# Performance work log

Hardware: AMD Instinct MI355X
Metric: run time of the kernel (lower is better)

Reference implementation:

```python
import math
import jax, jax.numpy as jnp
import numpy as np

B, K, D, R = 8192, 64, 128, 8
EPSILON = 1.0  # alpha_scale, used as diffusion epsilon


def setup_inputs() -> dict:
    key = jax.random.key(0)
    k1, k2, k3 = jax.random.split(key, 3)
    y = jax.random.normal(k1, (B, D), dtype=jnp.float32)
    m = 0.2 * jax.random.normal(k2, (K, D), dtype=jnp.float32)          # init_mean_scale=0.2
    delta = jnp.full((K, D), -2.0, dtype=jnp.float32)                    # init_delta=-2.0
    U = 0.001 * jax.random.normal(k3, (K, D, R), dtype=jnp.float32)
    # log_alpha_raw = alpha_scale * log(ones(K)/K)
    log_alpha_raw = jnp.full((K,), math.log(1.0 / K), dtype=jnp.float32)
    return {"y": y, "m": m, "delta": delta, "U": U, "log_alpha_raw": log_alpha_raw}


def reference(y, m, delta, U, log_alpha_raw):
    """log z_theta(y) = logsumexp_k [log_alpha_k + log N(y; m_k, eps*S_k)],
    S_k = diag(exp(delta_k)) + U_k U_k^T, solved via Woodbury + Cholesky."""
    d = y.shape[-1]
    eps = jnp.asarray(EPSILON, y.dtype)
    log_alpha = (log_alpha_raw - jnp.mean(log_alpha_raw)) / EPSILON

    S_diag = jnp.exp(delta)            # [K, d]
    S_inv = 1.0 / S_diag               # [K, d]

    # Capacitance M_k = I_r + U_k^T diag(S_inv_k) U_k, Cholesky L_k
    V = S_inv[..., None] * U                              # [K, d, r]
    Mcap = jnp.eye(R, dtype=y.dtype) + jnp.einsum('kdr,kds->krs', U, V)  # [K, r, r]
    L = jnp.linalg.cholesky(Mcap)                         # [K, r, r]
    logdet_S = jnp.sum(jnp.log(S_diag), axis=-1) \
        + 2.0 * jnp.sum(jnp.log(jnp.diagonal(L, axis1=-2, axis2=-1)), axis=-1)  # [K]

    diff = y[:, None, :] - m[None, :, :]                  # [B, K, d]
    u1 = diff * S_inv[None]                               # [B, K, d]
    # Woodbury correction: solve M_k s = U_k^T u1 for all (b, k)
    t = jnp.einsum('kdr,bkd->krb', U, u1)                 # [K, r, B] (B as multiple RHS)
    z1 = jax.scipy.linalg.solve_triangular(L, t, lower=True)
    s = jax.scipy.linalg.solve_triangular(jnp.swapaxes(L, -1, -2), z1, lower=False)  # [K, r, B]
    Us = jnp.einsum('kdr,krb->bkd', U, s)                 # [B, K, d]
    S_inv_diff = u1 - Us * S_inv[None]                    # [B, K, d]

    quad = jnp.sum(diff * S_inv_diff, axis=-1)            # [B, K]
    log_norm = 0.5 * (d * (math.log(2.0 * math.pi) + jnp.log(eps)) + logdet_S)  # [K]
    logits = log_alpha[None, :] - 0.5 * quad / eps - log_norm[None, :]          # [B, K]
    return jax.scipy.special.logsumexp(logits, axis=-1)   # [B]
```

## Files before the change

### kernel.cpp

```cpp
#include <hip/hip_runtime.h>
#include <math.h>

#define D_DIM 128
#define K_DIM 64
#define R_DIM 8
#define B_DIM 8192
#define KG    4
#define ESTR  161
#define TCH   5120

#define WS_C0F   81920
#define WS_PARTF 81984
#define WS_XGF   147520

typedef __bf16 bf16x8 __attribute__((ext_vector_type(8)));
typedef float  f32x4  __attribute__((ext_vector_type(4)));

static __device__ inline unsigned short f2bf(float f) {
  union { float f; unsigned int u; } v; v.f = f;
  unsigned int u = v.u;
  unsigned int lsb = (u >> 16) & 1;
  u += 0x7fffu + lsb;
  return (unsigned short)(u >> 16);
}

__global__ __launch_bounds__(128) void precomp_kernel(
    const float* __restrict__ m, const float* __restrict__ delta,
    const float* __restrict__ U, const float* __restrict__ lar,
    float* __restrict__ ws) {
  const int k = blockIdx.x;
  const int d = threadIdx.x;

  __shared__ float U_l[D_DIM][R_DIM];
  __shared__ float V_l[D_DIM][R_DIM];
  __shared__ float W_l[D_DIM][R_DIM];
  __shared__ float m_l[D_DIM];
  __shared__ float red[64];
  __shared__ float Linv_s[R_DIM][R_DIM];
  __shared__ float q_s[R_DIM];
  __shared__ float c0_s[1];
  __shared__ float redA[D_DIM], redB[D_DIM], redC[D_DIM];

  const float dl    = delta[k * D_DIM + d];
  const float s_inv = expf(-dl);
  const float mv    = m[k * D_DIM + d];
  m_l[d] = mv;
  const float* Up = U + (size_t)(k * D_DIM + d) * R_DIM;
#pragma unroll
  for (int r = 0; r < R_DIM; ++r) {
    float u = Up[r];
    U_l[d][r] = u;
    V_l[d][r] = u * s_inv;
  }
  redA[d] = dl;
  redB[d] = mv * mv * s_inv;
  redC[d] = (d < K_DIM) ? lar[d] : 0.f;
  __syncthreads();

  if (d < 64) {
    const int r = d >> 3, s = d & 7;
    float acc = (r == s) ? 1.0f : 0.0f;
#pragma unroll 8
    for (int dd = 0; dd < D_DIM; ++dd) acc += U_l[dd][r] * V_l[dd][s];
    red[d] = acc;
  }
  __syncthreads();

  for (int off = 64; off > 0; off >>= 1) {
    if (d < off) {
      redA[d] += redA[d + off];
      redB[d] += redB[d + off];
      redC[d] += redC[d + off];
    }
    __syncthreads();
  }

  if (d == 0) {
    float Lm[8][8];
#pragma unroll
    for (int i = 0; i < 8; ++i) {
#pragma unroll
      for (int j = 0; j < 8; ++j) {
        if (j > i) continue;
        float sum = red[i * 8 + j];
#pragma unroll
        for (int p = 0; p < 8; ++p)
          if (p < j) sum -= Lm[i][p] * Lm[j][p];
        if (i == j) Lm[i][i] = sqrtf(sum);
        else        Lm[i][j] = sum / Lm[j][j];
      }
    }
    float ld = 0.f;
#pragma unroll
    for (int i = 0; i < 8; ++i) ld += logf(Lm[i][i]);

    float Li[8][8];
#pragma unroll
    for (int i = 0; i < 8; ++i)
#pragma unroll
      for (int j = 0; j < 8; ++j) Li[i][j] = 0.f;
#pragma unroll
    for (int j = 0; j < 8; ++j) {
      Li[j][j] = 1.0f / Lm[j][j];
#pragma unroll
      for (int i = 0; i < 8; ++i) {
        if (i <= j) continue;
        float sum = 0.f;
#pragma unroll
        for (int p = 0; p < 8; ++p)
          if (p >= j && p < i) sum += Lm[i][p] * Li[p][j];
        Li[i][j] = -sum / Lm[i][i];
      }
    }
#pragma unroll
    for (int i = 0; i < 8; ++i)
#pragma unroll
      for (int j = 0; j < 8; ++j) Linv_s[i][j] = Li[i][j];

    const float mean = redC[0] * (1.0f / K_DIM);
    const float log_alpha = lar[k] - mean;
    const float logdetS = redA[0] + 2.0f * ld;
    const float LOG2PI = 1.8378770664093453f;
    const float log_norm = 0.5f * ((float)D_DIM * LOG2PI + logdetS);
    c0_s[0] = log_alpha - log_norm - 0.5f * redB[0];
  }
  __syncthreads();

  float Wr[R_DIM];
#pragma unroll
  for (int r = 0; r < R_DIM; ++r) {
    float acc = 0.f;
#pragma unroll
    for (int s2 = 0; s2 < R_DIM; ++s2)
      if (s2 <= r) acc += V_l[d][s2] * Linv_s[r][s2];
    Wr[r] = acc;
    W_l[d][r] = acc;
  }
  __syncthreads();

  if (d < R_DIM) {
    float acc = 0.f;
#pragma unroll 8
    for (int dd = 0; dd < D_DIM; ++dd) acc += W_l[dd][d] * m_l[dd];
    q_s[d] = acc;
  }
  __syncthreads();

  float hp = mv * s_inv;
#pragma unroll
  for (int r = 0; r < R_DIM; ++r) hp -= q_s[r] * Wr[r];

  const float INV_SQRT2 = 0.70710678118654752f;
  unsigned short* T = (unsigned short*)ws;
  const int kg = k >> 4, kl = k & 15;
  const int chunk = d >> 5, pos = d & 31;
  const size_t base_y = (((size_t)kg * 8 + chunk) * 160) * 32;
  const size_t base_q = (((size_t)kg * 8 + 4 + chunk) * 160) * 32;
#pragma unroll
  for (int c = 0; c < 8; ++c) {
    T[base_y + (size_t)(kl * 10 + c) * 32 + pos] = f2bf(Wr[c] * INV_SQRT2);
    T[base_q + (size_t)(kl * 10 + c) * 32 + pos] = 0;
  }
  T[base_y + (size_t)(kl * 10 + 8) * 32 + pos] = f2bf(hp);
  T[base_q + (size_t)(kl * 10 + 8) * 32 + pos] = f2bf(-0.5f * s_inv);
  T[base_y + (size_t)(kl * 10 + 9) * 32 + pos] = 0;
  T[base_q + (size_t)(kl * 10 + 9) * 32 + pos] = 0;

  if (d == 0) {
    float qq = 0.f;
#pragma unroll
    for (int r = 0; r < R_DIM; ++r) qq += q_s[r] * q_s[r];
    ws[WS_C0F + k] = c0_s[0] + 0.5f * qq;
  }
}

__global__ __launch_bounds__(256) void x_prep_kernel(
    const float* __restrict__ y, float* __restrict__ ws) {
  const int i   = blockIdx.x * 256 + threadIdx.x;
  const int row = i >> 5;
  const int seg = i & 31;
  const float4* ya = (const float4*)y + (size_t)row * 32 + (seg & 15) * 2;
  float4 a = ya[0], b = ya[1];
  if (seg >= 16) {
    a.x *= a.x; a.y *= a.y; a.z *= a.z; a.w *= a.w;
    b.x *= b.x; b.y *= b.y; b.z *= b.z; b.w *= b.w;
  }
  union { unsigned short us[8]; uint4 v; } o;
  o.us[0] = f2bf(a.x); o.us[1] = f2bf(a.y); o.us[2] = f2bf(a.z); o.us[3] = f2bf(a.w);
  o.us[4] = f2bf(b.x); o.us[5] = f2bf(b.y); o.us[6] = f2bf(b.z); o.us[7] = f2bf(b.w);
  uint4* xg = (uint4*)(ws + WS_XGF);
  xg[(size_t)row * 32 + (seg ^ (row & 31))] = o.v;
}

__global__ __launch_bounds__(256, 4) void logz_main(
    const float* __restrict__ ws, float* __restrict__ part) {
  __shared__ __align__(16) unsigned short sX[32 * 256];
  __shared__ __align__(16) float sbuf[32 * ESTR];
  __shared__ float vals2[32 * 17];

  const int tid   = threadIdx.x;
  const int lane  = tid & 63;
  const int wv    = tid >> 6;
  const int wr    = wv >> 1;
  const int wc    = wv & 1;
  const int col_l = lane & 15;
  const int quad  = lane >> 4;
  const int rt    = (int)blockIdx.x >> 2;
  const int kg    = (int)blockIdx.x & 3;

  {
    const float* xsrc = ws + WS_XGF + (size_t)rt * 4096;
#pragma unroll
    for (int j = 0; j < 4; ++j) {
      const int off = (wv * 4 + j) * 256;
      __builtin_amdgcn_global_load_lds(
          (const __attribute__((address_space(1))) void*)(xsrc + off + lane * 4),
          (__attribute__((address_space(3))) void*)((float*)sX + off),
          16, 0, 0);
    }
  }

  f32x4 acc[5];
#pragma unroll
  for (int f = 0; f < 5; ++f) { acc[f][0] = 0.f; acc[f][1] = 0.f; acc[f][2] = 0.f; acc[f][3] = 0.f; }

  const float* tG = ws + (size_t)kg * 8 * (TCH / 2);
  unsigned short* sT = (unsigned short*)sbuf;
  const int rowA = wr * 16 + col_l;

  for (int pair = 0; pair < 4; ++pair) {
    if (pair) __syncthreads();
    {
      const float* src = tG + (size_t)pair * TCH;
#pragma unroll
      for (int j = 0; j < 5; ++j) {
        const int off = (wv * 5 + j) * 256;
        __builtin_amdgcn_global_load_lds(
            (const __attribute__((address_space(1))) void*)(src + off + lane * 4),
            (__attribute__((address_space(3))) void*)((float*)sbuf + off),
            16, 0, 0);
      }
    }
    __syncthreads();
#pragma unroll
    for (int ii = 0; ii < 2; ++ii) {
      const int kiter = pair * 2 + ii;
      const bf16x8 a = *(const bf16x8*)(sX + ((size_t)rowA * 32
                          + (((kiter * 4 + quad) ^ rowA) & 31)) * 8);
      const unsigned short* cb = sT + ii * TCH;
#pragma unroll
      for (int f = 0; f < 5; ++f) {
        const bf16x8 b = *(const bf16x8*)(cb + (wc * 80 + f * 16 + col_l) * 32
                                             + quad * 8);
        acc[f] = __builtin_amdgcn_mfma_f32_16x16x32_bf16(a, b, acc[f], 0, 0, 0);
      }
    }
  }

  __syncthreads();
  float* evals = sbuf;
#pragma unroll
  for (int f = 0; f < 5; ++f) {
    const int col = wc * 80 + f * 16 + col_l;
    const int c10 = col % 10;
#pragma unroll
    for (int reg = 0; reg < 4; ++reg) {
      const float v = acc[f][reg];
      evals[(wr * 16 + quad * 4 + reg) * ESTR + col] = (c10 == 8) ? v : v * v;
    }
  }
  __syncthreads();

  const float* c0p = ws + WS_C0F + kg * 16;
#pragma unroll
  for (int j = 0; j < 2; ++j) {
    const int idx = tid + j * 256;
    const int row = idx >> 4, kl = idx & 15;
    const float* e = evals + row * ESTR + kl * 10;
    float s = c0p[kl] + e[8];
#pragma unroll
    for (int c = 0; c < 8; ++c) s += e[c];
    vals2[row * 17 + kl] = s;
  }
  __syncthreads();

  if (tid < 32) {
    const int row = tid;
    float mx = -INFINITY;
#pragma unroll
    for (int j = 0; j < 16; ++j) mx = fmaxf(mx, vals2[row * 17 + j]);
    float s = 0.f;
#pragma unroll
    for (int j = 0; j < 16; ++j) s += expf(vals2[row * 17 + j] - mx);
    *(float2*)(part + ((size_t)(rt * 32 + row) * KG + kg) * 2) = make_float2(mx, s);
  }
}

__global__ __launch_bounds__(256) void reduce_kernel(
    const float* __restrict__ part, float* __restrict__ out) {
  const int b = blockIdx.x * 256 + threadIdx.x;
  const float4 a0 = ((const float4*)part)[b * 2];
  const float4 a1 = ((const float4*)part)[b * 2 + 1];
  float mx = fmaxf(fmaxf(a0.x, a0.z), fmaxf(a1.x, a1.z));
  float s = a0.y * expf(a0.x - mx) + a0.w * expf(a0.z - mx)
          + a1.y * expf(a1.x - mx) + a1.w * expf(a1.z - mx);
  out[b] = mx + logf(s);
}

extern "C" void kernel_launch(void* const* d_in, const int* in_sizes, int n_in,
                              void* d_out, int out_size, void* d_ws, size_t ws_size,
                              hipStream_t stream) {
  const float* y     = (const float*)d_in[0];
  const float* m     = (const float*)d_in[1];
  const float* delta = (const float*)d_in[2];
  const float* U     = (const float*)d_in[3];
  const float* lar   = (const float*)d_in[4];
  float* out = (float*)d_out;
  float* ws  = (float*)d_ws;

  precomp_kernel<<<K_DIM, 128, 0, stream>>>(m, delta, U, lar, ws);
  x_prep_kernel<<<B_DIM * 32 / 256, 256, 0, stream>>>(y, ws);
  logz_main<<<(B_DIM / 32) * KG, 256, 0, stream>>>(ws, ws + WS_PARTF);
  reduce_kernel<<<B_DIM / 256, 256, 0, stream>>>(ws + WS_PARTF, out);
}
```

Measured before the change: 84.81 us.

## Fuse x-prep, main GEMM and logsumexp reduction into one kernel

```diff
diff --git a/kernel.cpp b/kernel.cpp
--- a/kernel.cpp
+++ b/kernel.cpp
@@ -5,13 +5,9 @@
 #define K_DIM 64
 #define R_DIM 8
 #define B_DIM 8192
-#define KG    4
-#define ESTR  161
-#define TCH   5120
+#define XSTR  264
 
 #define WS_C0F   81920
-#define WS_PARTF 81984
-#define WS_XGF   147520
 
 typedef __bf16 bf16x8 __attribute__((ext_vector_type(8)));
 typedef float  f32x4  __attribute__((ext_vector_type(4)));
@@ -174,137 +170,129 @@
   }
 }
 
-__global__ __launch_bounds__(256) void x_prep_kernel(
-    const float* __restrict__ y, float* __restrict__ ws) {
-  const int i   = blockIdx.x * 256 + threadIdx.x;
-  const int row = i >> 5;
-  const int seg = i & 31;
-  const float4* ya = (const float4*)y + (size_t)row * 32 + (seg & 15) * 2;
-  float4 a = ya[0], b = ya[1];
-  if (seg >= 16) {
-    a.x *= a.x; a.y *= a.y; a.z *= a.z; a.w *= a.w;
-    b.x *= b.x; b.y *= b.y; b.z *= b.z; b.w *= b.w;
-  }
-  union { unsigned short us[8]; uint4 v; } o;
-  o.us[0] = f2bf(a.x); o.us[1] = f2bf(a.y); o.us[2] = f2bf(a.z); o.us[3] = f2bf(a.w);
-  o.us[4] = f2bf(b.x); o.us[5] = f2bf(b.y); o.us[6] = f2bf(b.z); o.us[7] = f2bf(b.w);
-  uint4* xg = (uint4*)(ws + WS_XGF);
-  xg[(size_t)row * 32 + (seg ^ (row & 31))] = o.v;
-}
-
-__global__ __launch_bounds__(256, 4) void logz_main(
-    const float* __restrict__ ws, float* __restrict__ part) {
-  __shared__ __align__(16) unsigned short sX[32 * 256];
-  __shared__ __align__(16) float sbuf[32 * ESTR];
-  __shared__ float vals2[32 * 17];
+__global__ __launch_bounds__(512, 1) void logz_full(
+    const float* __restrict__ y, const float* __restrict__ ws,
+    float* __restrict__ out) {
+  __shared__ __align__(16) char smem[16896 + 81920];
+  __shared__ float vals2[32 * 65];
+
+  unsigned short* sX = (unsigned short*)smem;
+  unsigned short* sT = (unsigned short*)(smem + 16896);
 
   const int tid   = threadIdx.x;
   const int lane  = tid & 63;
   const int wv    = tid >> 6;
-  const int wr    = wv >> 1;
-  const int wc    = wv & 1;
+  const int wr    = wv & 1;
+  const int wc    = wv >> 1;
   const int col_l = lane & 15;
   const int quad  = lane >> 4;
-  const int rt    = (int)blockIdx.x >> 2;
-  const int kg    = (int)blockIdx.x & 3;
+  const int r0    = (int)blockIdx.x * 32;
+
+  const int kg_m = wv >> 1;
+  const int wi5  = (wv & 1) * 5;
 
   {
-    const float* xsrc = ws + WS_XGF + (size_t)rt * 4096;
-#pragma unroll
-    for (int j = 0; j < 4; ++j) {
-      const int off = (wv * 4 + j) * 256;
+#pragma unroll
+    for (int j = 0; j < 5; ++j) {
+      const int within = wi5 + j;
+      const float* src = ws + (size_t)kg_m * 20480 + 0 * 2560 + within * 256;
       __builtin_amdgcn_global_load_lds(
-          (const __attribute__((address_space(1))) void*)(xsrc + off + lane * 4),
-          (__attribute__((address_space(3))) void*)((float*)sX + off),
+          (const __attribute__((address_space(1))) void*)(src + lane * 4),
+          (__attribute__((address_space(3))) void*)(sT + kg_m * 5120 + within * 512),
           16, 0, 0);
     }
   }
 
-  f32x4 acc[5];
-#pragma unroll
-  for (int f = 0; f < 5; ++f) { acc[f][0] = 0.f; acc[f][1] = 0.f; acc[f][2] = 0.f; acc[f][3] = 0.f; }
-
-  const float* tG = ws + (size_t)kg * 8 * (TCH / 2);
-  unsigned short* sT = (unsigned short*)sbuf;
+  {
+#pragma unroll
+    for (int j = 0; j < 2; ++j) {
+      const int idx = tid + j * 512;
+      const int row = idx >> 5, g = idx & 31;
+      const float4* ya = (const float4*)y + (size_t)(r0 + row) * 32 + (g & 15) * 2;
+      float4 a = ya[0], b = ya[1];
+      if (g >= 16) {
+        a.x *= a.x; a.y *= a.y; a.z *= a.z; a.w *= a.w;
+        b.x *= b.x; b.y *= b.y; b.z *= b.z; b.w *= b.w;
+      }
+      union { unsigned short us[8]; uint4 v; } o;
+      o.us[0] = f2bf(a.x); o.us[1] = f2bf(a.y); o.us[2] = f2bf(a.z); o.us[3] = f2bf(a.w);
+      o.us[4] = f2bf(b.x); o.us[5] = f2bf(b.y); o.us[6] = f2bf(b.z); o.us[7] = f2bf(b.w);
+      *(uint4*)(sX + row * XSTR + g * 8) = o.v;
+    }
+  }
+
+  f32x4 acc[10];
+#pragma unroll
+  for (int f = 0; f < 10; ++f) { acc[f][0] = 0.f; acc[f][1] = 0.f; acc[f][2] = 0.f; acc[f][3] = 0.f; }
+
   const int rowA = wr * 16 + col_l;
 
-  for (int pair = 0; pair < 4; ++pair) {
-    if (pair) __syncthreads();
-    {
-      const float* src = tG + (size_t)pair * TCH;
+  for (int c = 0; c < 8; ++c) {
+    __syncthreads();
+    if (c < 7) {
+      const int nb = (c + 1) & 1;
 #pragma unroll
       for (int j = 0; j < 5; ++j) {
-        const int off = (wv * 5 + j) * 256;
+        const int within = wi5 + j;
+        const float* src = ws + (size_t)kg_m * 20480 + (c + 1) * 2560 + within * 256;
         __builtin_amdgcn_global_load_lds(
-            (const __attribute__((address_space(1))) void*)(src + off + lane * 4),
-            (__attribute__((address_space(3))) void*)((float*)sbuf + off),
+            (const __attribute__((address_space(1))) void*)(src + lane * 4),
+            (__attribute__((address_space(3))) void*)(sT + nb * 20480 + kg_m * 5120 + within * 512),
             16, 0, 0);
       }
     }
-    __syncthreads();
-#pragma unroll
-    for (int ii = 0; ii < 2; ++ii) {
-      const int kiter = pair * 2 + ii;
-      const bf16x8 a = *(const bf16x8*)(sX + ((size_t)rowA * 32
-                          + (((kiter * 4 + quad) ^ rowA) & 31)) * 8);
-      const unsigned short* cb = sT + ii * TCH;
-#pragma unroll
-      for (int f = 0; f < 5; ++f) {
-        const bf16x8 b = *(const bf16x8*)(cb + (wc * 80 + f * 16 + col_l) * 32
-                                             + quad * 8);
-        acc[f] = __builtin_amdgcn_mfma_f32_16x16x32_bf16(a, b, acc[f], 0, 0, 0);
-      }
-    }
-  }
-
-  __syncthreads();
-  float* evals = sbuf;
-#pragma unroll
-  for (int f = 0; f < 5; ++f) {
-    const int col = wc * 80 + f * 16 + col_l;
-    const int c10 = col % 10;
+    const bf16x8 a = *(const bf16x8*)(sX + rowA * XSTR + c * 32 + quad * 8);
+    const unsigned short* tb = sT + (c & 1) * 20480 + wc * 5120;
+#pragma unroll
+    for (int f = 0; f < 10; ++f) {
+      const bf16x8 b = *(const bf16x8*)(tb + (f * 16 + col_l) * 32 + quad * 8);
+      acc[f] = __builtin_amdgcn_mfma_f32_16x16x32_bf16(a, b, acc[f], 0, 0, 0);
+    }
+  }
+
+  __syncthreads();
+  float* evals = (float*)smem;
+#pragma unroll
+  for (int f = 0; f < 10; ++f) {
+    const int c_in = f * 16 + col_l;
+    const int c10  = c_in % 10;
+    const int col  = wc * 160 + c_in;
 #pragma unroll
     for (int reg = 0; reg < 4; ++reg) {
+      const int row = wr * 16 + quad * 4 + reg;
       const float v = acc[f][reg];
-      evals[(wr * 16 + quad * 4 + reg) * ESTR + col] = (c10 == 8) ? v : v * v;
-    }
-  }
-  __syncthreads();
-
-  const float* c0p = ws + WS_C0F + kg * 16;
-#pragma unroll
-  for (int j = 0; j < 2; ++j) {
-    const int idx = tid + j * 256;
-    const int row = idx >> 4, kl = idx & 15;
-    const float* e = evals + row * ESTR + kl * 10;
+      evals[row * 640 + col] = (c10 == 8) ? v : v * v;
+    }
+  }
+  __syncthreads();
+
+  const float* c0p = ws + WS_C0F;
+#pragma unroll
+  for (int j = 0; j < 4; ++j) {
+    const int idx = tid + j * 512;
+    const int row = idx >> 6, kl = idx & 63;
+    const float* e = evals + row * 640 + kl * 10;
     float s = c0p[kl] + e[8];
 #pragma unroll
     for (int c = 0; c < 8; ++c) s += e[c];
-    vals2[row * 17 + kl] = s;
-  }
-  __syncthreads();
-
-  if (tid < 32) {
-    const int row = tid;
-    float mx = -INFINITY;
-#pragma unroll
-    for (int j = 0; j < 16; ++j) mx = fmaxf(mx, vals2[row * 17 + j]);
-    float s = 0.f;
-#pragma unroll
-    for (int j = 0; j < 16; ++j) s += expf(vals2[row * 17 + j] - mx);
-    *(float2*)(part + ((size_t)(rt * 32 + row) * KG + kg) * 2) = make_float2(mx, s);
-  }
-}
-
-__global__ __launch_bounds__(256) void reduce_kernel(
-    const float* __restrict__ part, float* __restrict__ out) {
-  const int b = blockIdx.x * 256 + threadIdx.x;
-  const float4 a0 = ((const float4*)part)[b * 2];
-  const float4 a1 = ((const float4*)part)[b * 2 + 1];
-  float mx = fmaxf(fmaxf(a0.x, a0.z), fmaxf(a1.x, a1.z));
-  float s = a0.y * expf(a0.x - mx) + a0.w * expf(a0.z - mx)
-          + a1.y * expf(a1.x - mx) + a1.w * expf(a1.z - mx);
-  out[b] = mx + logf(s);
+    vals2[row * 65 + kl] = s;
+  }
+  __syncthreads();
+
+#pragma unroll
+  for (int rr = 0; rr < 4; ++rr) {
+    const int row = wv * 4 + rr;
+    const float val = vals2[row * 65 + lane];
+    float mx = val;
+#pragma unroll
+    for (int off = 1; off < 64; off <<= 1)
+      mx = fmaxf(mx, __shfl_xor(mx, off, 64));
+    float ex = expf(val - mx);
+#pragma unroll
+    for (int off = 1; off < 64; off <<= 1)
+      ex += __shfl_xor(ex, off, 64);
+    if (lane == 0) out[r0 + row] = mx + logf(ex);
+  }
 }
 
 extern "C" void kernel_launch(void* const* d_in, const int* in_sizes, int n_in,
@@ -319,7 +307,5 @@
   float* ws  = (float*)d_ws;
 
   precomp_kernel<<<K_DIM, 128, 0, stream>>>(m, delta, U, lar, ws);
-  x_prep_kernel<<<B_DIM * 32 / 256, 256, 0, stream>>>(y, ws);
-  logz_main<<<(B_DIM / 32) * KG, 256, 0, stream>>>(ws, ws + WS_PARTF);
-  reduce_kernel<<<B_DIM / 256, 256, 0, stream>>>(ws + WS_PARTF, out);
+  logz_full<<<B_DIM / 32, 512, 0, stream>>>(y, ws, out);
 }
```

After: 80.37 us. 5.2% less time.
